# Performance work log

Hardware: AMD Instinct MI355X
Metric: run time of the kernel (lower is better)

The kernel has to match this reference:

```python
import jax, jax.numpy as jnp
import numpy as np

B, S, HID = 1, 4096, 3584
NH, NKV, HD = 16, 8, 256
Q_SIZE, KV_SIZE = NH * HD, NKV * HD
SCALE = 256.0 ** -0.5          # query_pre_attn_scalar ** -0.5
SOFTCAP = 50.0                 # attn_logit_softcapping
WINDOW = 2048 - 1              # effective sliding window (sliding_window - 1)
THETA = 10000.0                # rope_theta
NEG = -1e30


def setup_inputs() -> dict:
    key = jax.random.key(0)
    k1, k2, k3 = jax.random.split(key, 3)
    hidden_states = jax.random.normal(k1, (B, S, HID), dtype=jnp.float32)
    position_ids = jnp.arange(S, dtype=jnp.int64).reshape(1, S)
    w_qkv = jax.random.normal(k2, (Q_SIZE + 2 * KV_SIZE, HID), dtype=jnp.float32) * 0.02
    w_o = jax.random.normal(k3, (HID, Q_SIZE), dtype=jnp.float32) * 0.02
    return {"position_ids": position_ids, "hidden_states": hidden_states,
            "w_qkv": w_qkv, "w_o": w_o}


def _rope_neox(x, pos):
    # x: [B, S, n_heads, HD]; pos: [B, S]
    half = HD // 2
    inv_freq = 1.0 / (THETA ** (jnp.arange(half, dtype=jnp.float32) * 2.0 / HD))
    ang = pos.astype(jnp.float32)[..., None] * inv_freq          # [B, S, half]
    cos = jnp.cos(ang)[:, :, None, :]                            # [B, S, 1, half]
    sin = jnp.sin(ang)[:, :, None, :]
    x1, x2 = x[..., :half], x[..., half:]
    return jnp.concatenate([x1 * cos - x2 * sin, x2 * cos + x1 * sin], axis=-1)


def reference(position_ids, hidden_states, w_qkv, w_o):
    # QKV projection (no bias)
    qkv = hidden_states @ w_qkv.T                                # [B, S, Q+2KV]
    q = qkv[..., :Q_SIZE].reshape(B, S, NH, HD)
    k = qkv[..., Q_SIZE:Q_SIZE + KV_SIZE].reshape(B, S, NKV, HD)
    v = qkv[..., Q_SIZE + KV_SIZE:].reshape(B, S, NKV, HD)

    # Neox-style RoPE over full head_dim
    q = _rope_neox(q, position_ids)
    k = _rope_neox(k, position_ids)

    # GQA: expand kv heads to query heads
    rep = NH // NKV
    k = jnp.repeat(k, rep, axis=2)                               # [B, S, NH, HD]
    v = jnp.repeat(v, rep, axis=2)

    # Scaled scores with tanh logit softcapping
    scores = jnp.einsum('bqhd,bkhd->bhqk', q, k) * SCALE
    scores = SOFTCAP * jnp.tanh(scores / SOFTCAP)

    # Causal + sliding-window mask: j <= i and i - j <= WINDOW
    i = jnp.arange(S)[:, None]
    j = jnp.arange(S)[None, :]
    mask = (j <= i) & (i - j <= WINDOW)                          # [S, S]
    scores = jnp.where(mask[None, None, :, :], scores, NEG)

    probs = jax.nn.softmax(scores, axis=-1)
    attn = jnp.einsum('bhqk,bkhd->bqhd', probs, v).reshape(B, S, Q_SIZE)

    # Output projection (no bias)
    return attn @ w_o.T                                          # [B, S, HID]
```

## Files before the change

kernel.cpp:

```cpp
#include <hip/hip_runtime.h>
#include <cstdint>
#include <cstddef>

#define S_LEN 4096
#define HID   3584
#define NH    16
#define NKV   8
#define HD    256
#define QSZ   (NH*HD)
#define KVSZ  (NKV*HD)
#define QKV_N (QSZ + 2*KVSZ)
#define WINDOW 2047

typedef unsigned short u16;
typedef __bf16 bf16x8 __attribute__((ext_vector_type(8)));
typedef u16    u16x8  __attribute__((ext_vector_type(8)));
typedef u16    u16x4  __attribute__((ext_vector_type(4)));
typedef float  f32x4  __attribute__((ext_vector_type(4)));

__device__ inline float bf2f(u16 u) {
    union { unsigned u; float f; } v; v.u = ((unsigned)u) << 16; return v.f;
}
__device__ inline u16 f2bf(float f) {
    union { float f; unsigned u; } v; v.f = f;
    return (u16)((v.u + 0x7FFF + ((v.u >> 16) & 1)) >> 16);
}
__device__ inline float fast_tanh(float x) {
    x = fminf(fmaxf(x, -20.f), 20.f);
    float e = __expf(2.f * x);
    return 1.f - 2.f / (e + 1.f);
}

__global__ __launch_bounds__(256)
void cast_f32_bf16(const float* __restrict__ src, u16* __restrict__ dst, int n4) {
    int i = blockIdx.x * blockDim.x + threadIdx.x;
    if (i >= n4) return;
    float4 v = ((const float4*)src)[i];
    u16x4 o;
    o[0] = f2bf(v.x); o[1] = f2bf(v.y); o[2] = f2bf(v.z); o[3] = f2bf(v.w);
    ((u16x4*)dst)[i] = o;
}

template<int BF16OUT>
__global__ __launch_bounds__(256)
void gemm_bt(const u16* __restrict__ A, const u16* __restrict__ B,
             void* __restrict__ Cv, int M, int N, int K) {
    __shared__ u16 lA[128 * 32];
    __shared__ u16 lB[128 * 32];
    const int tid  = threadIdx.x;
    const int lane = tid & 63, wave = tid >> 6;
    const int quad = lane >> 4, l16 = lane & 15;
    const int m0 = blockIdx.y * 128, n0 = blockIdx.x * 128;
    const int wm = (wave & 1) * 64, wn = (wave >> 1) * 64;

    f32x4 zero = {0.f, 0.f, 0.f, 0.f};
    f32x4 acc[4][4];
#pragma unroll
    for (int i = 0; i < 4; ++i)
#pragma unroll
        for (int j = 0; j < 4; ++j) acc[i][j] = zero;

    const int c0 = tid, c1 = tid + 256;
    const int r0 = c0 >> 2, cc0 = (c0 & 3) * 8;
    const int r1 = c1 >> 2, cc1 = (c1 & 3) * 8;
    const u16* A0 = A + (size_t)(m0 + r0) * K + cc0;
    const u16* A1 = A + (size_t)(m0 + r1) * K + cc1;
    const u16* B0 = B + (size_t)(n0 + r0) * K + cc0;
    const u16* B1 = B + (size_t)(n0 + r1) * K + cc1;

    u16x8 ra0 = *(const u16x8*)A0;
    u16x8 ra1 = *(const u16x8*)A1;
    u16x8 rb0 = *(const u16x8*)B0;
    u16x8 rb1 = *(const u16x8*)B1;

    for (int k0 = 0; k0 < K; k0 += 32) {
        __syncthreads();
        *(u16x8*)(&lA[c0 * 8]) = ra0;
        *(u16x8*)(&lA[c1 * 8]) = ra1;
        *(u16x8*)(&lB[c0 * 8]) = rb0;
        *(u16x8*)(&lB[c1 * 8]) = rb1;
        __syncthreads();
        int kn = k0 + 32;
        if (kn < K) {
            ra0 = *(const u16x8*)(A0 + kn);
            ra1 = *(const u16x8*)(A1 + kn);
            rb0 = *(const u16x8*)(B0 + kn);
            rb1 = *(const u16x8*)(B1 + kn);
        }
        bf16x8 af[4], bfr[4];
#pragma unroll
        for (int mt = 0; mt < 4; ++mt)
            af[mt] = *(const bf16x8*)(&lA[(wm + mt * 16 + l16) * 32 + quad * 8]);
#pragma unroll
        for (int nt = 0; nt < 4; ++nt)
            bfr[nt] = *(const bf16x8*)(&lB[(wn + nt * 16 + l16) * 32 + quad * 8]);
#pragma unroll
        for (int mt = 0; mt < 4; ++mt)
#pragma unroll
            for (int nt = 0; nt < 4; ++nt)
                acc[mt][nt] = __builtin_amdgcn_mfma_f32_16x16x32_bf16(
                    af[mt], bfr[nt], acc[mt][nt], 0, 0, 0);
    }

#pragma unroll
    for (int mt = 0; mt < 4; ++mt)
#pragma unroll
        for (int nt = 0; nt < 4; ++nt)
#pragma unroll
            for (int r = 0; r < 4; ++r) {
                int row = m0 + wm + mt * 16 + quad * 4 + r;
                int col = n0 + wn + nt * 16 + l16;
                float v = acc[mt][nt][r];
                if (BF16OUT) ((u16*)Cv)[(size_t)row * N + col] = f2bf(v);
                else         ((float*)Cv)[(size_t)row * N + col] = v;
            }
}

__global__ __launch_bounds__(256)
void rope_split(const u16* __restrict__ qkv, u16* __restrict__ Qb,
                u16* __restrict__ Kb, u16* __restrict__ Vb) {
    const int s = blockIdx.x;
    const int t = threadIdx.x;
    const float pos = (float)s;
    const u16* row = qkv + (size_t)s * QKV_N;

    for (int p = t; p < 2048; p += 256) {
        int h = p >> 7, d = p & 127;
        float inv = __expf(-(float)d * 0.0719557841560639f);
        float ang = pos * inv, sn, cs;
        sincosf(ang, &sn, &cs);
        float x1 = bf2f(row[h * HD + d]);
        float x2 = bf2f(row[h * HD + d + 128]);
        size_t base = ((size_t)h * S_LEN + s) * HD;
        Qb[base + d]       = f2bf((x1 * cs - x2 * sn) * 0.0625f);
        Qb[base + d + 128] = f2bf((x2 * cs + x1 * sn) * 0.0625f);
    }
    for (int p = t; p < 1024; p += 256) {
        int h = p >> 7, d = p & 127;
        float inv = __expf(-(float)d * 0.0719557841560639f);
        float ang = pos * inv, sn, cs;
        sincosf(ang, &sn, &cs);
        float x1 = bf2f(row[QSZ + h * HD + d]);
        float x2 = bf2f(row[QSZ + h * HD + d + 128]);
        size_t base = ((size_t)h * S_LEN + s) * HD;
        Kb[base + d]       = f2bf(x1 * cs - x2 * sn);
        Kb[base + d + 128] = f2bf(x2 * cs + x1 * sn);
    }
    for (int e = t; e < 2048; e += 256) {
        int h = e >> 8, d = e & 255;
        Vb[((size_t)h * S_LEN + s) * HD + d] = row[QSZ + KVSZ + e];
    }
}

__global__ __launch_bounds__(256)
void attn_fused(const u16* __restrict__ Qb, const u16* __restrict__ Kb,
                const u16* __restrict__ Vb, u16* __restrict__ O) {
    const int h  = blockIdx.y;
    const int qt = blockIdx.x;
    const int hkv = h >> 1;
    const int qbase = qt * 64;
    const int tid = threadIdx.x, wave = tid >> 6, lane = tid & 63;
    const int quad = lane >> 4, l16 = lane & 15;

    __shared__ u16 lK[32 * 264];
    __shared__ u16 lV[256 * 40];
    __shared__ u16 lP[4][16 * 40];

    const int qrow = qbase + wave * 16 + l16;
    bf16x8 qf[8];
    {
        const u16* qp = Qb + ((size_t)h * S_LEN + qrow) * HD + quad * 8;
#pragma unroll
        for (int f = 0; f < 8; ++f) qf[f] = *(const bf16x8*)(qp + f * 32);
    }

    f32x4 zero = {0.f, 0.f, 0.f, 0.f};
    f32x4 o[16];
#pragma unroll
    for (int i = 0; i < 16; ++i) o[i] = zero;
    float m_r[4], l_r[4];
#pragma unroll
    for (int r = 0; r < 4; ++r) { m_r[r] = -1e4f; l_r[r] = 0.f; }

    const int t0 = max(0, qbase - WINDOW) >> 5;
    const int t1 = (qbase + 63) >> 5;
    const u16* Kh = Kb + (size_t)hkv * S_LEN * HD;
    const u16* Vh = Vb + (size_t)hkv * S_LEN * HD;

    for (int kt = t0; kt <= t1; ++kt) {
        const int kb = kt * 32;
        __syncthreads();
#pragma unroll
        for (int it = 0; it < 4; ++it) {
            int c = tid + it * 256;
            int krow = c >> 5;
            int col = (c & 31) * 8;
            *(u16x8*)(&lK[krow * 264 + col]) =
                *(const u16x8*)(Kh + (size_t)(kb + krow) * HD + col);
        }
        {
            int key = tid & 31;
            int db0 = (tid >> 5) * 8;
#pragma unroll
            for (int it = 0; it < 4; ++it) {
                int dbase = db0 + it * 64;
                u16x8 v = *(const u16x8*)(Vh + (size_t)(kb + key) * HD + dbase);
#pragma unroll
                for (int j = 0; j < 8; ++j) lV[(dbase + j) * 40 + key] = v[j];
            }
        }
        __syncthreads();

        f32x4 sc[2];
#pragma unroll
        for (int ct = 0; ct < 2; ++ct) {
            f32x4 a = zero;
#pragma unroll
            for (int f = 0; f < 8; ++f) {
                bf16x8 kf = *(const bf16x8*)(&lK[(ct * 16 + l16) * 264 + f * 32 + quad * 8]);
                a = __builtin_amdgcn_mfma_f32_16x16x32_bf16(qf[f], kf, a, 0, 0, 0);
            }
            sc[ct] = a;
        }

        float p0[4], p1[4], rowmax[4];
#pragma unroll
        for (int r = 0; r < 4; ++r) {
            const int gi = qbase + wave * 16 + quad * 4 + r;
            float x0 = 50.f * fast_tanh(sc[0][r] * 0.02f);
            float x1 = 50.f * fast_tanh(sc[1][r] * 0.02f);
            int gj0 = kb + l16, gj1 = kb + 16 + l16;
            bool ok0 = (gj0 <= gi) && (gi - gj0 <= WINDOW);
            bool ok1 = (gj1 <= gi) && (gi - gj1 <= WINDOW);
            p0[r] = ok0 ? x0 : -1e30f;
            p1[r] = ok1 ? x1 : -1e30f;
            rowmax[r] = fmaxf(p0[r], p1[r]);
        }
#pragma unroll
        for (int m = 1; m < 16; m <<= 1)
#pragma unroll
            for (int r = 0; r < 4; ++r)
                rowmax[r] = fmaxf(rowmax[r], __shfl_xor(rowmax[r], m, 64));

        float al[4], rs[4];
#pragma unroll
        for (int r = 0; r < 4; ++r) {
            float mn = fmaxf(m_r[r], rowmax[r]);
            al[r] = __expf(m_r[r] - mn);
            m_r[r] = mn;
            float e0 = __expf(p0[r] - mn);
            float e1 = __expf(p1[r] - mn);
            p0[r] = e0; p1[r] = e1;
            rs[r] = e0 + e1;
        }
#pragma unroll
        for (int m = 1; m < 16; m <<= 1)
#pragma unroll
            for (int r = 0; r < 4; ++r)
                rs[r] += __shfl_xor(rs[r], m, 64);

        u16* pw = &lP[wave][0];
#pragma unroll
        for (int r = 0; r < 4; ++r) {
            l_r[r] = l_r[r] * al[r] + rs[r];
            pw[(quad * 4 + r) * 40 + l16]      = f2bf(p0[r]);
            pw[(quad * 4 + r) * 40 + 16 + l16] = f2bf(p1[r]);
        }
#pragma unroll
        for (int dt = 0; dt < 16; ++dt)
#pragma unroll
            for (int r = 0; r < 4; ++r) o[dt][r] *= al[r];

        asm volatile("s_waitcnt lgkmcnt(0)" ::: "memory");
        bf16x8 pf = *(const bf16x8*)(&pw[l16 * 40 + quad * 8]);
#pragma unroll
        for (int dt = 0; dt < 16; ++dt) {
            bf16x8 vf = *(const bf16x8*)(&lV[(dt * 16 + l16) * 40 + quad * 8]);
            o[dt] = __builtin_amdgcn_mfma_f32_16x16x32_bf16(pf, vf, o[dt], 0, 0, 0);
        }
    }

    float inv_l[4];
#pragma unroll
    for (int r = 0; r < 4; ++r) inv_l[r] = 1.f / l_r[r];
#pragma unroll
    for (int dt = 0; dt < 16; ++dt)
#pragma unroll
        for (int r = 0; r < 4; ++r) {
            int grow = qbase + wave * 16 + quad * 4 + r;
            int gcol = h * HD + dt * 16 + l16;
            O[(size_t)grow * QSZ + gcol] = f2bf(o[dt][r] * inv_l[r]);
        }
}

extern "C" void kernel_launch(void* const* d_in, const int* in_sizes, int n_in,
                              void* d_out, int out_size, void* d_ws, size_t ws_size,
                              hipStream_t stream) {
    const float* hidden = (const float*)d_in[1];
    const float* w_qkv  = (const float*)d_in[2];
    const float* w_o    = (const float*)d_in[3];
    float* out = (float*)d_out;

    char* ws = (char*)d_ws;
    size_t off = 0;
    auto alloc = [&](size_t bytes) {
        void* p = ws + off; off += (bytes + 255) & ~(size_t)255; return p;
    };
    u16* Xb    = (u16*)alloc((size_t)S_LEN * HID   * 2);
    u16* Wqkvb = (u16*)alloc((size_t)QKV_N * HID   * 2);
    u16* QKVb  = (u16*)alloc((size_t)S_LEN * QKV_N * 2);
    u16* Qb    = (u16*)alloc((size_t)NH  * S_LEN * HD * 2);
    u16* Kb    = (u16*)alloc((size_t)NKV * S_LEN * HD * 2);
    u16* Vb    = (u16*)alloc((size_t)NKV * S_LEN * HD * 2);
    u16* attn  = QKVb;
    u16* Wob   = Xb;

    const int n1 = S_LEN * HID / 4;
    const int n2 = QKV_N * HID / 4;

    cast_f32_bf16<<<dim3((n1 + 255) / 256), dim3(256), 0, stream>>>(hidden, Xb, n1);
    cast_f32_bf16<<<dim3((n2 + 255) / 256), dim3(256), 0, stream>>>(w_qkv, Wqkvb, n2);
    gemm_bt<1><<<dim3(QKV_N / 128, S_LEN / 128), dim3(256), 0, stream>>>(
        Xb, Wqkvb, (void*)QKVb, S_LEN, QKV_N, HID);
    rope_split<<<dim3(S_LEN), dim3(256), 0, stream>>>(QKVb, Qb, Kb, Vb);
    cast_f32_bf16<<<dim3((n1 + 255) / 256), dim3(256), 0, stream>>>(w_o, Wob, n1);
    attn_fused<<<dim3(S_LEN / 64, NH), dim3(256), 0, stream>>>(Qb, Kb, Vb, attn);
    gemm_bt<0><<<dim3(HID / 128, S_LEN / 128), dim3(256), 0, stream>>>(
        attn, Wob, (void*)out, S_LEN, HID, QSZ);
}
```

Before: 1.185 ms.

## Restructure attention with 128-query tiles, pre-transposed V and fixed-offset softmax

Attention blocks now process 128 queries, with two 16-row tiles per wave, so each K/V tile loaded into LDS is reused across twice as many rows. V is transposed once by a new kernel so tiles can be copied straight into LDS with global_load_lds, and K loads are register-prefetched. Because softcapping bounds the logits at 50, the running-max rescaling is replaced by a fixed-offset exponential, and tiles fully outside a wave's window are skipped. The GEMM also switches to direct global-to-LDS loads but drops its register prefetch, which may expose memory latency there.

After: 1.277 ms. 7.7% more time.

```diff
diff --git a/kernel.cpp b/kernel.cpp
--- a/kernel.cpp
+++ b/kernel.cpp
@@ -25,10 +25,12 @@
     union { float f; unsigned u; } v; v.f = f;
     return (u16)((v.u + 0x7FFF + ((v.u >> 16) & 1)) >> 16);
 }
-__device__ inline float fast_tanh(float x) {
-    x = fminf(fmaxf(x, -20.f), 20.f);
-    float e = __expf(2.f * x);
-    return 1.f - 2.f / (e + 1.f);
+
+__device__ inline void gl_lds16(const void* g, void* l) {
+    __builtin_amdgcn_global_load_lds(
+        (const __attribute__((address_space(1))) void*)g,
+        (__attribute__((address_space(3))) void*)l,
+        16, 0, 0);
 }
 
 __global__ __launch_bounds__(256)
@@ -53,6 +55,14 @@
     const int m0 = blockIdx.y * 128, n0 = blockIdx.x * 128;
     const int wm = (wave & 1) * 64, wn = (wave >> 1) * 64;
 
+    const int c0 = wave * 128 + lane, c1 = c0 + 64;
+    const u16* gA0 = A + (size_t)(m0 + (c0 >> 2)) * K + (c0 & 3) * 8;
+    const u16* gA1 = A + (size_t)(m0 + (c1 >> 2)) * K + (c1 & 3) * 8;
+    const u16* gB0 = B + (size_t)(n0 + (c0 >> 2)) * K + (c0 & 3) * 8;
+    const u16* gB1 = B + (size_t)(n0 + (c1 >> 2)) * K + (c1 & 3) * 8;
+    char* lA0 = (char*)lA + wave * 2048;
+    char* lB0 = (char*)lB + wave * 2048;
+
     f32x4 zero = {0.f, 0.f, 0.f, 0.f};
     f32x4 acc[4][4];
 #pragma unroll
@@ -60,33 +70,14 @@
 #pragma unroll
         for (int j = 0; j < 4; ++j) acc[i][j] = zero;
 
-    const int c0 = tid, c1 = tid + 256;
-    const int r0 = c0 >> 2, cc0 = (c0 & 3) * 8;
-    const int r1 = c1 >> 2, cc1 = (c1 & 3) * 8;
-    const u16* A0 = A + (size_t)(m0 + r0) * K + cc0;
-    const u16* A1 = A + (size_t)(m0 + r1) * K + cc1;
-    const u16* B0 = B + (size_t)(n0 + r0) * K + cc0;
-    const u16* B1 = B + (size_t)(n0 + r1) * K + cc1;
-
-    u16x8 ra0 = *(const u16x8*)A0;
-    u16x8 ra1 = *(const u16x8*)A1;
-    u16x8 rb0 = *(const u16x8*)B0;
-    u16x8 rb1 = *(const u16x8*)B1;
-
     for (int k0 = 0; k0 < K; k0 += 32) {
         __syncthreads();
-        *(u16x8*)(&lA[c0 * 8]) = ra0;
-        *(u16x8*)(&lA[c1 * 8]) = ra1;
-        *(u16x8*)(&lB[c0 * 8]) = rb0;
-        *(u16x8*)(&lB[c1 * 8]) = rb1;
+        gl_lds16(gA0 + k0, lA0);
+        gl_lds16(gA1 + k0, lA0 + 1024);
+        gl_lds16(gB0 + k0, lB0);
+        gl_lds16(gB1 + k0, lB0 + 1024);
         __syncthreads();
-        int kn = k0 + 32;
-        if (kn < K) {
-            ra0 = *(const u16x8*)(A0 + kn);
-            ra1 = *(const u16x8*)(A1 + kn);
-            rb0 = *(const u16x8*)(B0 + kn);
-            rb1 = *(const u16x8*)(B1 + kn);
-        }
+
         bf16x8 af[4], bfr[4];
 #pragma unroll
         for (int mt = 0; mt < 4; ++mt)
@@ -153,144 +144,175 @@
 }
 
 __global__ __launch_bounds__(256)
+void vtrans(const u16* __restrict__ Vb, u16* __restrict__ Vt) {
+    const int s0 = blockIdx.x * 64, d0 = blockIdx.y * 64, h = blockIdx.z;
+    __shared__ u16 t[64][72];
+    const int tid = threadIdx.x;
+    const u16* src = Vb + (size_t)h * S_LEN * HD;
+#pragma unroll
+    for (int c = tid; c < 512; c += 256) {
+        int sr = c >> 3, dc = (c & 7) * 8;
+        *(u16x8*)&t[sr][dc] = *(const u16x8*)(src + (size_t)(s0 + sr) * HD + d0 + dc);
+    }
+    __syncthreads();
+    u16* dst = Vt + (size_t)h * HD * S_LEN;
+#pragma unroll
+    for (int c = tid; c < 512; c += 256) {
+        int sc8 = (c & 7) * 8, dd = c >> 3;
+        u16x8 v;
+#pragma unroll
+        for (int j = 0; j < 8; ++j) v[j] = t[sc8 + j][dd];
+        *(u16x8*)(dst + (size_t)(d0 + dd) * S_LEN + s0 + sc8) = v;
+    }
+}
+
+__global__ __launch_bounds__(256, 2)
 void attn_fused(const u16* __restrict__ Qb, const u16* __restrict__ Kb,
-                const u16* __restrict__ Vb, u16* __restrict__ O) {
+                const u16* __restrict__ Vt, u16* __restrict__ O) {
     const int h  = blockIdx.y;
     const int qt = blockIdx.x;
     const int hkv = h >> 1;
-    const int qbase = qt * 64;
+    const int qbase = qt * 128;
     const int tid = threadIdx.x, wave = tid >> 6, lane = tid & 63;
     const int quad = lane >> 4, l16 = lane & 15;
 
     __shared__ u16 lK[32 * 264];
-    __shared__ u16 lV[256 * 40];
-    __shared__ u16 lP[4][16 * 40];
-
-    const int qrow = qbase + wave * 16 + l16;
-    bf16x8 qf[8];
-    {
-        const u16* qp = Qb + ((size_t)h * S_LEN + qrow) * HD + quad * 8;
-#pragma unroll
-        for (int f = 0; f < 8; ++f) qf[f] = *(const bf16x8*)(qp + f * 32);
+    __shared__ u16 lV[256 * 32];
+    __shared__ u16 lP[4][2][16 * 40];
+
+    const int wlo = qbase + wave * 32;
+    const int whi = wlo + 31;
+
+    bf16x8 qf[2][8];
+#pragma unroll
+    for (int rt = 0; rt < 2; ++rt) {
+        const u16* qp = Qb + ((size_t)h * S_LEN + wlo + rt * 16 + l16) * HD + quad * 8;
+#pragma unroll
+        for (int f = 0; f < 8; ++f) qf[rt][f] = *(const bf16x8*)(qp + f * 32);
     }
 
     f32x4 zero = {0.f, 0.f, 0.f, 0.f};
-    f32x4 o[16];
-#pragma unroll
-    for (int i = 0; i < 16; ++i) o[i] = zero;
-    float m_r[4], l_r[4];
-#pragma unroll
-    for (int r = 0; r < 4; ++r) { m_r[r] = -1e4f; l_r[r] = 0.f; }
+    f32x4 o[2][16];
+#pragma unroll
+    for (int rt = 0; rt < 2; ++rt)
+#pragma unroll
+        for (int dt = 0; dt < 16; ++dt) o[rt][dt] = zero;
+    float l_r[2][4];
+#pragma unroll
+    for (int rt = 0; rt < 2; ++rt)
+#pragma unroll
+        for (int r = 0; r < 4; ++r) l_r[rt][r] = 0.f;
 
     const int t0 = max(0, qbase - WINDOW) >> 5;
-    const int t1 = (qbase + 63) >> 5;
+    const int t1 = (qbase + 127) >> 5;
     const u16* Kh = Kb + (size_t)hkv * S_LEN * HD;
-    const u16* Vh = Vb + (size_t)hkv * S_LEN * HD;
+    const u16* Vh = Vt + (size_t)hkv * HD * S_LEN;
+
+    const u16* kbase[4];
+    int lkoff[4];
+#pragma unroll
+    for (int it = 0; it < 4; ++it) {
+        int c = tid + it * 256;
+        kbase[it] = Kh + (size_t)(c >> 5) * HD + (c & 31) * 8;
+        lkoff[it] = (c >> 5) * 264 + (c & 31) * 8;
+    }
+    const u16* vbase[4];
+#pragma unroll
+    for (int j = 0; j < 4; ++j) {
+        int c = wave * 256 + j * 64 + lane;
+        vbase[j] = Vh + (size_t)(c >> 2) * S_LEN + (c & 3) * 8;
+    }
+    char* lVw = (char*)lV + wave * 4096;
+
+    u16x8 kreg[4];
+    const int kb0 = t0 * 32;
+#pragma unroll
+    for (int it = 0; it < 4; ++it)
+        kreg[it] = *(const u16x8*)(kbase[it] + (size_t)kb0 * HD);
 
     for (int kt = t0; kt <= t1; ++kt) {
         const int kb = kt * 32;
         __syncthreads();
 #pragma unroll
-        for (int it = 0; it < 4; ++it) {
-            int c = tid + it * 256;
-            int krow = c >> 5;
-            int col = (c & 31) * 8;
-            *(u16x8*)(&lK[krow * 264 + col]) =
-                *(const u16x8*)(Kh + (size_t)(kb + krow) * HD + col);
+        for (int j = 0; j < 4; ++j)
+            gl_lds16(vbase[j] + kb, lVw + j * 1024);
+#pragma unroll
+        for (int it = 0; it < 4; ++it)
+            *(u16x8*)(&lK[lkoff[it]]) = kreg[it];
+        __syncthreads();
+        if (kt < t1) {
+#pragma unroll
+            for (int it = 0; it < 4; ++it)
+                kreg[it] = *(const u16x8*)(kbase[it] + (size_t)(kb + 32) * HD);
         }
-        {
-            int key = tid & 31;
-            int db0 = (tid >> 5) * 8;
-#pragma unroll
-            for (int it = 0; it < 4; ++it) {
-                int dbase = db0 + it * 64;
-                u16x8 v = *(const u16x8*)(Vh + (size_t)(kb + key) * HD + dbase);
-#pragma unroll
-                for (int j = 0; j < 8; ++j) lV[(dbase + j) * 40 + key] = v[j];
+        bool active = (kb <= whi) && (kb + 31 >= wlo - WINDOW);
+        if (!active) continue;
+
+        f32x4 sc[2][2];
+        sc[0][0] = zero; sc[0][1] = zero; sc[1][0] = zero; sc[1][1] = zero;
+#pragma unroll
+        for (int ct = 0; ct < 2; ++ct)
+#pragma unroll
+            for (int f = 0; f < 8; ++f) {
+                bf16x8 kf = *(const bf16x8*)(&lK[(ct * 16 + l16) * 264 + f * 32 + quad * 8]);
+                sc[0][ct] = __builtin_amdgcn_mfma_f32_16x16x32_bf16(qf[0][f], kf, sc[0][ct], 0, 0, 0);
+                sc[1][ct] = __builtin_amdgcn_mfma_f32_16x16x32_bf16(qf[1][f], kf, sc[1][ct], 0, 0, 0);
+            }
+
+        u16* pw0 = &lP[wave][0][0];
+        u16* pw1 = &lP[wave][1][0];
+#pragma unroll
+        for (int rt = 0; rt < 2; ++rt) {
+            u16* pw = rt ? pw1 : pw0;
+#pragma unroll
+            for (int r = 0; r < 4; ++r) {
+                const int gi = wlo + rt * 16 + quad * 4 + r;
+#pragma unroll
+                for (int ct = 0; ct < 2; ++ct) {
+                    const int gj = kb + ct * 16 + l16;
+                    float s = sc[rt][ct][r];
+                    float u = __expf(s * 0.04f);
+                    float p = __expf(-100.f / (u + 1.f));
+                    bool ok = (gj <= gi) && (gi - gj <= WINDOW);
+                    p = ok ? p : 0.f;
+                    l_r[rt][r] += p;
+                    pw[(quad * 4 + r) * 40 + ct * 16 + l16] = f2bf(p);
+                }
             }
         }
-        __syncthreads();
-
-        f32x4 sc[2];
-#pragma unroll
-        for (int ct = 0; ct < 2; ++ct) {
-            f32x4 a = zero;
-#pragma unroll
-            for (int f = 0; f < 8; ++f) {
-                bf16x8 kf = *(const bf16x8*)(&lK[(ct * 16 + l16) * 264 + f * 32 + quad * 8]);
-                a = __builtin_amdgcn_mfma_f32_16x16x32_bf16(qf[f], kf, a, 0, 0, 0);
+        asm volatile("s_waitcnt lgkmcnt(0)" ::: "memory");
+        bf16x8 pf0 = *(const bf16x8*)(&pw0[l16 * 40 + quad * 8]);
+        bf16x8 pf1 = *(const bf16x8*)(&pw1[l16 * 40 + quad * 8]);
+#pragma unroll
+        for (int dt = 0; dt < 16; ++dt) {
+            bf16x8 vf = *(const bf16x8*)(&lV[(dt * 16 + l16) * 32 + quad * 8]);
+            o[0][dt] = __builtin_amdgcn_mfma_f32_16x16x32_bf16(pf0, vf, o[0][dt], 0, 0, 0);
+            o[1][dt] = __builtin_amdgcn_mfma_f32_16x16x32_bf16(pf1, vf, o[1][dt], 0, 0, 0);
+        }
+    }
+
+    float inv_l[2][4];
+#pragma unroll
+    for (int rt = 0; rt < 2; ++rt)
+#pragma unroll
+        for (int r = 0; r < 4; ++r) {
+            float v = l_r[rt][r];
+            v += __shfl_xor(v, 1, 64);
+            v += __shfl_xor(v, 2, 64);
+            v += __shfl_xor(v, 4, 64);
+            v += __shfl_xor(v, 8, 64);
+            inv_l[rt][r] = 1.f / v;
+        }
+#pragma unroll
+    for (int rt = 0; rt < 2; ++rt)
+#pragma unroll
+        for (int dt = 0; dt < 16; ++dt)
+#pragma unroll
+            for (int r = 0; r < 4; ++r) {
+                int grow = wlo + rt * 16 + quad * 4 + r;
+                int gcol = h * HD + dt * 16 + l16;
+                O[(size_t)grow * QSZ + gcol] = f2bf(o[rt][dt][r] * inv_l[rt][r]);
             }
-            sc[ct] = a;
-        }
-
-        float p0[4], p1[4], rowmax[4];
-#pragma unroll
-        for (int r = 0; r < 4; ++r) {
-            const int gi = qbase + wave * 16 + quad * 4 + r;
-            float x0 = 50.f * fast_tanh(sc[0][r] * 0.02f);
-            float x1 = 50.f * fast_tanh(sc[1][r] * 0.02f);
-            int gj0 = kb + l16, gj1 = kb + 16 + l16;
-            bool ok0 = (gj0 <= gi) && (gi - gj0 <= WINDOW);
-            bool ok1 = (gj1 <= gi) && (gi - gj1 <= WINDOW);
-            p0[r] = ok0 ? x0 : -1e30f;
-            p1[r] = ok1 ? x1 : -1e30f;
-            rowmax[r] = fmaxf(p0[r], p1[r]);
-        }
-#pragma unroll
-        for (int m = 1; m < 16; m <<= 1)
-#pragma unroll
-            for (int r = 0; r < 4; ++r)
-                rowmax[r] = fmaxf(rowmax[r], __shfl_xor(rowmax[r], m, 64));
-
-        float al[4], rs[4];
-#pragma unroll
-        for (int r = 0; r < 4; ++r) {
-            float mn = fmaxf(m_r[r], rowmax[r]);
-            al[r] = __expf(m_r[r] - mn);
-            m_r[r] = mn;
-            float e0 = __expf(p0[r] - mn);
-            float e1 = __expf(p1[r] - mn);
-            p0[r] = e0; p1[r] = e1;
-            rs[r] = e0 + e1;
-        }
-#pragma unroll
-        for (int m = 1; m < 16; m <<= 1)
-#pragma unroll
-            for (int r = 0; r < 4; ++r)
-                rs[r] += __shfl_xor(rs[r], m, 64);
-
-        u16* pw = &lP[wave][0];
-#pragma unroll
-        for (int r = 0; r < 4; ++r) {
-            l_r[r] = l_r[r] * al[r] + rs[r];
-            pw[(quad * 4 + r) * 40 + l16]      = f2bf(p0[r]);
-            pw[(quad * 4 + r) * 40 + 16 + l16] = f2bf(p1[r]);
-        }
-#pragma unroll
-        for (int dt = 0; dt < 16; ++dt)
-#pragma unroll
-            for (int r = 0; r < 4; ++r) o[dt][r] *= al[r];
-
-        asm volatile("s_waitcnt lgkmcnt(0)" ::: "memory");
-        bf16x8 pf = *(const bf16x8*)(&pw[l16 * 40 + quad * 8]);
-#pragma unroll
-        for (int dt = 0; dt < 16; ++dt) {
-            bf16x8 vf = *(const bf16x8*)(&lV[(dt * 16 + l16) * 40 + quad * 8]);
-            o[dt] = __builtin_amdgcn_mfma_f32_16x16x32_bf16(pf, vf, o[dt], 0, 0, 0);
-        }
-    }
-
-    float inv_l[4];
-#pragma unroll
-    for (int r = 0; r < 4; ++r) inv_l[r] = 1.f / l_r[r];
-#pragma unroll
-    for (int dt = 0; dt < 16; ++dt)
-#pragma unroll
-        for (int r = 0; r < 4; ++r) {
-            int grow = qbase + wave * 16 + quad * 4 + r;
-            int gcol = h * HD + dt * 16 + l16;
-            O[(size_t)grow * QSZ + gcol] = f2bf(o[dt][r] * inv_l[r]);
-        }
 }
 
 extern "C" void kernel_launch(void* const* d_in, const int* in_sizes, int n_in,
@@ -312,6 +334,7 @@
     u16* Qb    = (u16*)alloc((size_t)NH  * S_LEN * HD * 2);
     u16* Kb    = (u16*)alloc((size_t)NKV * S_LEN * HD * 2);
     u16* Vb    = (u16*)alloc((size_t)NKV * S_LEN * HD * 2);
+    u16* Vt    = Wqkvb;
     u16* attn  = QKVb;
     u16* Wob   = Xb;
 
@@ -323,8 +346,9 @@
     gemm_bt<1><<<dim3(QKV_N / 128, S_LEN / 128), dim3(256), 0, stream>>>(
         Xb, Wqkvb, (void*)QKVb, S_LEN, QKV_N, HID);
     rope_split<<<dim3(S_LEN), dim3(256), 0, stream>>>(QKVb, Qb, Kb, Vb);
+    vtrans<<<dim3(S_LEN / 64, HD / 64, NKV), dim3(256), 0, stream>>>(Vb, Vt);
     cast_f32_bf16<<<dim3((n1 + 255) / 256), dim3(256), 0, stream>>>(w_o, Wob, n1);
-    attn_fused<<<dim3(S_LEN / 64, NH), dim3(256), 0, stream>>>(Qb, Kb, Vb, attn);
+    attn_fused<<<dim3(S_LEN / 128, NH), dim3(256), 0, stream>>>(Qb, Kb, Vt, attn);
     gemm_bt<0><<<dim3(HID / 128, S_LEN / 128), dim3(256), 0, stream>>>(
         attn, Wob, (void*)out, S_LEN, HID, QSZ);
 }
```
